# Optimization experiments

Hardware: AMD Instinct MI355X
Metric: run time of the kernel (lower is better)

## Reference

```python
import jax, jax.numpy as jnp
import numpy as np
import math

HIDDEN, HEADS, D_K = 768, 12, 64
BS, SEQ = 4, 2048


def setup_inputs() -> dict:
    key = jax.random.key(0)
    ks = jax.random.split(key, 5)
    s = 1.0 / math.sqrt(HIDDEN)
    return {
        "x": jax.random.normal(ks[0], (BS, SEQ, HIDDEN), dtype=jnp.float32),
        "Wq": jax.random.normal(ks[1], (HIDDEN, HIDDEN), dtype=jnp.float32) * s,
        "bq": jnp.zeros((HIDDEN,), jnp.float32),
        "Wk": jax.random.normal(ks[2], (HIDDEN, HIDDEN), dtype=jnp.float32) * s,
        "bk": jnp.zeros((HIDDEN,), jnp.float32),
        "Wv": jax.random.normal(ks[3], (HIDDEN, HIDDEN), dtype=jnp.float32) * s,
        "bv": jnp.zeros((HIDDEN,), jnp.float32),
        "Wo": jax.random.normal(ks[4], (HIDDEN, HIDDEN), dtype=jnp.float32) * s,
        "bo": jnp.zeros((HIDDEN,), jnp.float32),
    }


def reference(x, Wq, bq, Wk, bk, Wv, bv, Wo, bo):
    bs, seq, _ = x.shape
    # projections; nn.Linear computes x @ W.T + b
    def proj(W, b):
        y = jnp.einsum("bsd,ed->bse", x, W) + b
        return y.reshape(bs, seq, HEADS, D_K).transpose(0, 2, 1, 3)  # [b,h,s,d]
    q, k, v = proj(Wq, bq), proj(Wk, bk), proj(Wv, bv)
    scores = jnp.einsum("bhqd,bhkd->bhqk", q, k) / jnp.sqrt(jnp.float32(D_K))
    attn = jax.nn.softmax(scores, axis=-1)  # dropout = 0 (eval)
    ctx = jnp.einsum("bhqk,bhkd->bhqd", attn, v)
    ctx = ctx.transpose(0, 2, 1, 3).reshape(bs, seq, HIDDEN)
    return jnp.einsum("bsd,ed->bse", ctx, Wo) + bo
```

## Files before the change

kernel.cpp:

```cpp
#include <hip/hip_runtime.h>
#include <hip/hip_bf16.h>

#define HID 768
#define NHEAD 12
#define DKH 64
#define BSZ 4
#define SEQ 2048
#define MTOT (BSZ*SEQ)
#define NBH (BSZ*NHEAD)

typedef __attribute__((ext_vector_type(8))) short   s16x8;
typedef __attribute__((ext_vector_type(8))) __bf16  bf16x8;
typedef __attribute__((ext_vector_type(4))) __bf16  bf16x4;
typedef __attribute__((ext_vector_type(4))) float   f32x4;

#define MFMA16x32(A,B,C) __builtin_amdgcn_mfma_f32_16x16x32_bf16((A),(B),(C),0,0,0)

__device__ __forceinline__ unsigned short f2bf(float f) {
  union { float f; unsigned int u; } a; a.f = f;
  return (unsigned short)((a.u + 0x7FFFu + ((a.u >> 16) & 1u)) >> 16);
}

__device__ __forceinline__ void gload_lds16(const unsigned short* g, unsigned short* l) {
  __builtin_amdgcn_global_load_lds((const __attribute__((address_space(1))) void*)g,
                                   (__attribute__((address_space(3))) void*)l, 16, 0, 0);
}

__global__ __launch_bounds__(256) void cvtall_kernel(const float* __restrict__ x,
                                                     const float* __restrict__ w0,
                                                     const float* __restrict__ w1,
                                                     const float* __restrict__ w2,
                                                     const float* __restrict__ w3,
                                                     unsigned short* __restrict__ xb,
                                                     unsigned short* __restrict__ wb) {
  const int bid = blockIdx.x;
  const float* src; unsigned short* dst; int off;
  if (bid < 6144) {
    src = x; dst = xb; off = bid * 1024;
  } else {
    const int t = bid - 6144;
    const int wi = t / 576;
    const int ro = t - wi * 576;
    src = (wi == 0) ? w0 : (wi == 1) ? w1 : (wi == 2) ? w2 : w3;
    dst = wb + (size_t)wi * HID * HID;
    off = ro * 1024;
  }
  const int i = off + threadIdx.x * 4;
  float4 v = *(const float4*)(src + i);
  ushort4 o;
  o.x = f2bf(v.x); o.y = f2bf(v.y); o.z = f2bf(v.z); o.w = f2bf(v.w);
  *(ushort4*)(dst + i) = o;
}

#define GEMM_STEP(CUR, KTN, DOPREF)                                         \
  {                                                                         \
    if (DOPREF) {                                                           \
      _Pragma("unroll")                                                     \
      for (int i = 0; i < 4; ++i) {                                         \
        const int c = wave * 4 + i;                                         \
        gload_lds16(Aptr + (size_t)(c*8 + sr) * HID + (KTN) + sc8,          \
                    As[(CUR)^1] + c*512);                                   \
      }                                                                     \
      _Pragma("unroll")                                                     \
      for (int i = 0; i < NB; ++i) {                                        \
        const int c = wave * NB + i;                                        \
        gload_lds16(Wptr + (size_t)(c*8 + sr) * HID + (KTN) + sc8,          \
                    Bs[(CUR)^1] + c*512);                                   \
      }                                                                     \
    }                                                                       \
    const char* ab = (const char*)As[CUR];                                  \
    const char* bb = (const char*)Bs[CUR];                                  \
    _Pragma("unroll")                                                       \
    for (int kk = 0; kk < 2; ++kk) {                                        \
      bf16x8 af[4], bfr[NB];                                                \
      _Pragma("unroll")                                                     \
      for (int mb = 0; mb < 4; ++mb) {                                      \
        const int r = wm + mb*16 + l16;                                     \
        af[mb] = *(const bf16x8*)(ab + r*128 + (((kk*4 + lg) ^ (l16 & 7)) << 4)); \
      }                                                                     \
      _Pragma("unroll")                                                     \
      for (int nb = 0; nb < NB; ++nb) {                                     \
        const int r = wn + nb*16 + l16;                                     \
        bfr[nb] = *(const bf16x8*)(bb + r*128 + (((kk*4 + lg) ^ (l16 & 7)) << 4)); \
      }                                                                     \
      _Pragma("unroll")                                                     \
      for (int mb = 0; mb < 4; ++mb)                                        \
        _Pragma("unroll")                                                   \
        for (int nb = 0; nb < NB; ++nb)                                     \
          acc[mb][nb] = MFMA16x32(af[mb], bfr[nb], acc[mb][nb]);            \
    }                                                                       \
    __syncthreads();                                                        \
  }

template<int MODE, int NB>
__global__ __launch_bounds__(256) void gemm_kernel(
    const unsigned short* __restrict__ A,
    const unsigned short* __restrict__ W,
    const float* __restrict__ bias0,
    const float* __restrict__ bias1,
    const float* __restrict__ bias2,
    void* __restrict__ out_raw,
    unsigned short* __restrict__ vtimg)
{
  __shared__ unsigned short As[2][128*64];
  __shared__ unsigned short Bs[2][NB*32*64];
  const int tid  = threadIdx.x;
  const int wave = tid >> 6, lane = tid & 63;
  const int l16  = lane & 15, lg = lane >> 4;
  const int f    = blockIdx.x;
  const int xcd  = f & 7, rr = f >> 3;
  const int bx   = xcd*8 + (rr & 7), by = rr >> 3;
  const int m0   = bx * 128, n0 = by * (NB*32);
  const int wm   = (wave & 1) * 64,  wn = (wave >> 1) * (NB*16);

  const f32x4 z4 = {0.f, 0.f, 0.f, 0.f};
  f32x4 acc[4][NB];
#pragma unroll
  for (int i = 0; i < 4; ++i)
#pragma unroll
    for (int j = 0; j < NB; ++j) acc[i][j] = z4;

  const int sr  = lane >> 3;
  const int sc8 = ((lane & 7) ^ sr) << 3;
  const unsigned short* Aptr = A + (size_t)m0 * HID;
  const unsigned short* Wptr = W + (size_t)n0 * HID;

#pragma unroll
  for (int i = 0; i < 4; ++i) {
    const int c = wave * 4 + i;
    gload_lds16(Aptr + (size_t)(c*8 + sr) * HID + sc8, As[0] + c*512);
  }
#pragma unroll
  for (int i = 0; i < NB; ++i) {
    const int c = wave * NB + i;
    gload_lds16(Wptr + (size_t)(c*8 + sr) * HID + sc8, Bs[0] + c*512);
  }
  __syncthreads();

#pragma unroll 1
  for (int tt = 0; tt < 6; ++tt) {
    GEMM_STEP(0, (2*tt+1)*64, true)
    GEMM_STEP(1, (2*tt+2)*64, (tt < 5))
  }

  if (MODE == 0) {
    unsigned short* out = (unsigned short*)out_raw;
    const float QSCALE = 0.18033688011112042f;
    const int which = (n0 + wn) / HID;
    if (which == 2) {
      const int h = (n0 + wn - 2*HID) >> 6;
#pragma unroll
      for (int nb = 0; nb < NB; ++nb) {
        const int d = nb*16 + l16;
        const float bias = bias2[h*64 + d];
#pragma unroll
        for (int mb = 0; mb < 4; ++mb) {
          const int m    = m0 + wm + mb*16 + lg*4;
          const int b    = m >> 11, s = m & (SEQ - 1);
          const int tile = s >> 6;
          const int slot = ((s & 63) >> 2) ^ l16;
          ushort4 w;
          w.x = f2bf(acc[mb][nb][0] + bias);
          w.y = f2bf(acc[mb][nb][1] + bias);
          w.z = f2bf(acc[mb][nb][2] + bias);
          w.w = f2bf(acc[mb][nb][3] + bias);
          *(ushort4*)(vtimg + ((((size_t)(b*NHEAD + h)*32 + tile)*64 + d)*64 + slot*4)) = w;
        }
      }
    } else {
      const float* bp  = (which == 0) ? bias0 : bias1;
      const float scl  = (which == 0) ? QSCALE : 1.0f;
      const int e_base = n0 + wn - which*HID;
#pragma unroll
      for (int nb = 0; nb < NB; ++nb) {
        const int e = e_base + nb*16 + l16;
        const float bias = bp[e];
        const int h = e >> 6, d = e & 63;
#pragma unroll
        for (int mb = 0; mb < 4; ++mb)
#pragma unroll
          for (int j = 0; j < 4; ++j) {
            const int m = m0 + wm + mb*16 + lg*4 + j;
            const int b = m >> 11, s = m & (SEQ - 1);
            const float v = (acc[mb][nb][j] + bias) * scl;
            out[((((size_t)which*BSZ + b)*NHEAD + h)*SEQ + s)*DKH + d] = f2bf(v);
          }
      }
    }
  } else {
    float* out = (float*)out_raw;
#pragma unroll
    for (int nb = 0; nb < NB; ++nb) {
      const int n = n0 + wn + nb*16 + l16;
      const float bias = bias0[n];
#pragma unroll
      for (int mb = 0; mb < 4; ++mb)
#pragma unroll
        for (int j = 0; j < 4; ++j) {
          const int m = m0 + wm + mb*16 + lg*4 + j;
          out[(size_t)m*HID + n] = acc[mb][nb][j] + bias;
        }
    }
  }
}

#define ATTN_STEP(CUR, DOPREF)                                              \
  {                                                                         \
    if (DOPREF) {                                                           \
      gload_lds16(kSrc0, Ks[(CUR)^1] + wave*1024);                          \
      gload_lds16(kSrc1, Ks[(CUR)^1] + wave*1024 + 512);                    \
      gload_lds16(vSrc0, Vs[(CUR)^1] + wave*1024);                          \
      gload_lds16(vSrc1, Vs[(CUR)^1] + wave*1024 + 512);                    \
      kSrc0 += 64*DKH; kSrc1 += 64*DKH; vSrc0 += 4096; vSrc1 += 4096;       \
    }                                                                       \
    const char* kb = (const char*)Ks[CUR];                                  \
    const char* vb = (const char*)Vs[CUR];                                  \
    f32x4 sc[2][4];                                                         \
    __builtin_amdgcn_s_setprio(1);                                          \
    _Pragma("unroll")                                                       \
    for (int nb = 0; nb < 4; ++nb) {                                        \
      bf16x8 kf0 = *(const bf16x8*)(kb + kbase0 + nb*2048);                 \
      bf16x8 kf1 = *(const bf16x8*)(kb + kbase1 + nb*2048);                 \
      f32x4 z0 = z4, z1 = z4;                                               \
      z0 = MFMA16x32(kf0, qf[0][0], z0);                                    \
      z0 = MFMA16x32(kf1, qf[0][1], z0);                                    \
      z1 = MFMA16x32(kf0, qf[1][0], z1);                                    \
      z1 = MFMA16x32(kf1, qf[1][1], z1);                                    \
      sc[0][nb] = z0; sc[1][nb] = z1;                                       \
    }                                                                       \
    __builtin_amdgcn_s_setprio(0);                                          \
    bf16x8 pa[2][2];                                                        \
    _Pragma("unroll")                                                       \
    for (int qa = 0; qa < 2; ++qa)                                          \
      _Pragma("unroll")                                                     \
      for (int nb = 0; nb < 4; ++nb)                                        \
        _Pragma("unroll")                                                   \
        for (int j = 0; j < 4; ++j)                                         \
          pa[qa][nb>>1][(nb&1)*4 + j] =                                     \
            (__bf16)__builtin_amdgcn_exp2f(sc[qa][nb][j]);                  \
    __builtin_amdgcn_s_setprio(1);                                          \
    csum[0] = MFMA16x32(pa[0][0], ones, csum[0]);                           \
    csum[0] = MFMA16x32(pa[0][1], ones, csum[0]);                           \
    csum[1] = MFMA16x32(pa[1][0], ones, csum[1]);                           \
    csum[1] = MFMA16x32(pa[1][1], ones, csum[1]);                           \
    _Pragma("unroll")                                                       \
    for (int db = 0; db < 4; ++db) {                                        \
      bf16x4 v00 = *(const bf16x4*)(vb + vbase0 + db*2048);                 \
      bf16x4 v01 = *(const bf16x4*)(vb + vbase1 + db*2048);                 \
      bf16x4 v10 = *(const bf16x4*)(vb + vbase2 + db*2048);                 \
      bf16x4 v11 = *(const bf16x4*)(vb + vbase3 + db*2048);                 \
      bf16x8 vf0 = __builtin_shufflevector(v00, v01, 0,1,2,3,4,5,6,7);      \
      bf16x8 vf1 = __builtin_shufflevector(v10, v11, 0,1,2,3,4,5,6,7);      \
      cacc[0][db] = MFMA16x32(pa[0][0], vf0, cacc[0][db]);                  \
      cacc[0][db] = MFMA16x32(pa[0][1], vf1, cacc[0][db]);                  \
      cacc[1][db] = MFMA16x32(pa[1][0], vf0, cacc[1][db]);                  \
      cacc[1][db] = MFMA16x32(pa[1][1], vf1, cacc[1][db]);                  \
    }                                                                       \
    __builtin_amdgcn_s_setprio(0);                                          \
    __syncthreads();                                                        \
  }

__global__ __launch_bounds__(256, 3) void attn_kernel(const unsigned short* __restrict__ qkv,
                                                      const unsigned short* __restrict__ vtimg,
                                                      unsigned short* __restrict__ ctx)
{
  __shared__ unsigned short Ks[2][64*64];
  __shared__ unsigned short Vs[2][64*64];
  const int tid  = threadIdx.x;
  const int wave = tid >> 6, lane = tid & 63;
  const int l16  = lane & 15, lg = lane >> 4;
  const int f   = blockIdx.x;
  const int xcd = f & 7, idx = f >> 3;
  const int bh  = xcd * 6 + (idx >> 4);
  const int qt  = idx & 15;
  const int b   = bh / NHEAD, h = bh - b * NHEAD;
  const int q0  = qt * 128 + wave * 32;

  const unsigned short* Qg = qkv + (size_t)bh * (SEQ*DKH);
  const unsigned short* Kg = qkv + (size_t)(NBH + bh) * (SEQ*DKH);

  const int srow  = lane >> 3;
  const int scolK = ((lane & 7) ^ srow) << 3;
  const unsigned short* kSrc0 = Kg + (size_t)(wave*16 + srow) * DKH + scolK;
  const unsigned short* kSrc1 = Kg + (size_t)(wave*16 + 8 + srow) * DKH + scolK;
  const unsigned short* vSrc0 = vtimg + ((size_t)bh*32*64 + wave*16 + srow) * 64 + (lane & 7) * 8;
  const unsigned short* vSrc1 = vSrc0 + 8*64;

  const int kbase0 = l16*128 + ((lg ^ (l16 & 7)) << 4);
  const int kbase1 = l16*128 + (((lg + 4) ^ (l16 & 7)) << 4);
  const int vbase0 = l16*128 + (((lg     ) ^ l16) << 3);
  const int vbase1 = l16*128 + (((lg +  4) ^ l16) << 3);
  const int vbase2 = l16*128 + (((lg +  8) ^ l16) << 3);
  const int vbase3 = l16*128 + (((lg + 12) ^ l16) << 3);

  bf16x8 qf[2][2];
#pragma unroll
  for (int qa = 0; qa < 2; ++qa) {
    qf[qa][0] = *(const bf16x8*)(Qg + (size_t)(q0 + qa*16 + l16)*DKH + lg*8);
    qf[qa][1] = *(const bf16x8*)(Qg + (size_t)(q0 + qa*16 + l16)*DKH + 32 + lg*8);
  }

  bf16x8 ones;
#pragma unroll
  for (int e = 0; e < 8; ++e) ones[e] = (__bf16)1.0f;

  const f32x4 z4 = {0.f,0.f,0.f,0.f};
  f32x4 cacc[2][4];
  f32x4 csum[2] = {z4, z4};
#pragma unroll
  for (int qa = 0; qa < 2; ++qa)
#pragma unroll
    for (int db = 0; db < 4; ++db) cacc[qa][db] = z4;

  gload_lds16(kSrc0, Ks[0] + wave*1024);
  gload_lds16(kSrc1, Ks[0] + wave*1024 + 512);
  gload_lds16(vSrc0, Vs[0] + wave*1024);
  gload_lds16(vSrc1, Vs[0] + wave*1024 + 512);
  kSrc0 += 64*DKH; kSrc1 += 64*DKH; vSrc0 += 4096; vSrc1 += 4096;
  __syncthreads();

#pragma unroll 1
  for (int tt = 0; tt < 16; ++tt) {
    ATTN_STEP(0, true)
    ATTN_STEP(1, (tt < 15))
  }

#pragma unroll
  for (int qa = 0; qa < 2; ++qa) {
    f32x4 inv;
#pragma unroll
    for (int j = 0; j < 4; ++j) inv[j] = 1.0f / csum[qa][j];
#pragma unroll
    for (int db = 0; db < 4; ++db)
#pragma unroll
      for (int j = 0; j < 4; ++j) {
        const int srow2 = q0 + qa*16 + lg*4 + j;
        ctx[((size_t)(b*SEQ + srow2))*HID + h*DKH + db*16 + l16] = f2bf(cacc[qa][db][j] * inv[j]);
      }
  }
}

extern "C" void kernel_launch(void* const* d_in, const int* in_sizes, int n_in,
                              void* d_out, int out_size, void* d_ws, size_t ws_size,
                              hipStream_t stream) {
  (void)in_sizes; (void)n_in; (void)out_size; (void)ws_size;
  const float* x  = (const float*)d_in[0];
  const float* Wq = (const float*)d_in[1];
  const float* bq = (const float*)d_in[2];
  const float* Wk = (const float*)d_in[3];
  const float* bk = (const float*)d_in[4];
  const float* Wv = (const float*)d_in[5];
  const float* bv = (const float*)d_in[6];
  const float* Wo = (const float*)d_in[7];
  const float* bo = (const float*)d_in[8];

  unsigned short* ws   = (unsigned short*)d_ws;
  unsigned short* Xb   = ws;
  unsigned short* Wqkv = Xb + (size_t)MTOT * HID;
  unsigned short* Wob  = Wqkv + (size_t)3 * HID * HID;
  unsigned short* qkvb = Wob + (size_t)HID * HID;
  unsigned short* vtb  = qkvb + (size_t)2 * NBH * SEQ * DKH;
  unsigned short* ctxb = Xb;

  cvtall_kernel<<<6144 + 4*576, 256, 0, stream>>>(x, Wq, Wk, Wv, Wo, Xb, Wqkv);

  gemm_kernel<0,4><<<1152, 256, 0, stream>>>(Xb, Wqkv, bq, bk, bv, qkvb, vtb);
  attn_kernel<<<768, 256, 0, stream>>>(qkvb, vtb, ctxb);
  gemm_kernel<1,2><<<768, 256, 0, stream>>>(ctxb, Wob, bo, nullptr, nullptr, d_out, nullptr);
}
```

Before: 126.8 us.

## Give QKV GEMM a triple-buffered K=32 pipeline with vmcnt-based waits

```diff
diff --git a/kernel.cpp b/kernel.cpp
--- a/kernel.cpp
+++ b/kernel.cpp
@@ -52,73 +52,208 @@
   *(ushort4*)(dst + i) = o;
 }
 
-#define GEMM_STEP(CUR, KTN, DOPREF)                                         \
-  {                                                                         \
-    if (DOPREF) {                                                           \
-      _Pragma("unroll")                                                     \
-      for (int i = 0; i < 4; ++i) {                                         \
-        const int c = wave * 4 + i;                                         \
-        gload_lds16(Aptr + (size_t)(c*8 + sr) * HID + (KTN) + sc8,          \
-                    As[(CUR)^1] + c*512);                                   \
-      }                                                                     \
-      _Pragma("unroll")                                                     \
-      for (int i = 0; i < NB; ++i) {                                        \
-        const int c = wave * NB + i;                                        \
-        gload_lds16(Wptr + (size_t)(c*8 + sr) * HID + (KTN) + sc8,          \
-                    Bs[(CUR)^1] + c*512);                                   \
-      }                                                                     \
-    }                                                                       \
-    const char* ab = (const char*)As[CUR];                                  \
-    const char* bb = (const char*)Bs[CUR];                                  \
+#define VM4 asm volatile("s_waitcnt vmcnt(4)" ::: "memory")
+#define VM0 asm volatile("s_waitcnt vmcnt(0)" ::: "memory")
+#define CFENCE asm volatile("" ::: "memory")
+
+#define G0_STAGE(BUF, KTN)                                                  \
     _Pragma("unroll")                                                       \
-    for (int kk = 0; kk < 2; ++kk) {                                        \
-      bf16x8 af[4], bfr[NB];                                                \
+    for (int i = 0; i < 2; ++i) {                                           \
+      const int c = wave * 2 + i;                                           \
+      gload_lds16(Aptr + (size_t)(c*16 + sr4) * HID + (KTN) + sc4,          \
+                  As[BUF] + c*512);                                         \
+      gload_lds16(Wptr + (size_t)(c*16 + sr4) * HID + (KTN) + sc4,          \
+                  Bs[BUF] + c*512);                                         \
+    }
+
+#define G0_COMPUTE(BUF)                                                     \
+    {                                                                       \
+      const char* ab = (const char*)As[BUF];                                \
+      const char* bb = (const char*)Bs[BUF];                                \
+      bf16x8 af[4], bfr[4];                                                 \
       _Pragma("unroll")                                                     \
       for (int mb = 0; mb < 4; ++mb) {                                      \
         const int r = wm + mb*16 + l16;                                     \
-        af[mb] = *(const bf16x8*)(ab + r*128 + (((kk*4 + lg) ^ (l16 & 7)) << 4)); \
-      }                                                                     \
-      _Pragma("unroll")                                                     \
-      for (int nb = 0; nb < NB; ++nb) {                                     \
+        af[mb] = *(const bf16x8*)(ab + r*64 + (((lg) ^ (r & 3)) << 4));     \
+      }                                                                     \
+      _Pragma("unroll")                                                     \
+      for (int nb = 0; nb < 4; ++nb) {                                      \
         const int r = wn + nb*16 + l16;                                     \
-        bfr[nb] = *(const bf16x8*)(bb + r*128 + (((kk*4 + lg) ^ (l16 & 7)) << 4)); \
+        bfr[nb] = *(const bf16x8*)(bb + r*64 + (((lg) ^ (r & 3)) << 4));    \
       }                                                                     \
       _Pragma("unroll")                                                     \
       for (int mb = 0; mb < 4; ++mb)                                        \
         _Pragma("unroll")                                                   \
-        for (int nb = 0; nb < NB; ++nb)                                     \
+        for (int nb = 0; nb < 4; ++nb)                                      \
           acc[mb][nb] = MFMA16x32(af[mb], bfr[nb], acc[mb][nb]);            \
-    }                                                                       \
-    __syncthreads();                                                        \
-  }
-
-template<int MODE, int NB>
-__global__ __launch_bounds__(256) void gemm_kernel(
+    }
+
+#define G0_STEP(BUF, KTN, PF)                                               \
+  {                                                                         \
+    if (PF) { G0_STAGE(((BUF)+2)%3, KTN) }                                  \
+    G0_COMPUTE(BUF)                                                         \
+    if (PF) { VM4; } else { VM0; }                                          \
+    __builtin_amdgcn_sched_barrier(0);                                      \
+    __builtin_amdgcn_s_barrier();                                           \
+    CFENCE;                                                                 \
+  }
+
+__global__ __launch_bounds__(256, 3) void gemm0_kernel(
     const unsigned short* __restrict__ A,
     const unsigned short* __restrict__ W,
     const float* __restrict__ bias0,
     const float* __restrict__ bias1,
     const float* __restrict__ bias2,
-    void* __restrict__ out_raw,
+    unsigned short* __restrict__ out,
     unsigned short* __restrict__ vtimg)
 {
-  __shared__ unsigned short As[2][128*64];
-  __shared__ unsigned short Bs[2][NB*32*64];
+  __shared__ unsigned short As[3][128*32];
+  __shared__ unsigned short Bs[3][128*32];
   const int tid  = threadIdx.x;
   const int wave = tid >> 6, lane = tid & 63;
   const int l16  = lane & 15, lg = lane >> 4;
   const int f    = blockIdx.x;
   const int xcd  = f & 7, rr = f >> 3;
   const int bx   = xcd*8 + (rr & 7), by = rr >> 3;
-  const int m0   = bx * 128, n0 = by * (NB*32);
-  const int wm   = (wave & 1) * 64,  wn = (wave >> 1) * (NB*16);
+  const int m0   = bx * 128, n0 = by * 128;
+  const int wm   = (wave & 1) * 64,  wn = (wave >> 1) * 64;
 
   const f32x4 z4 = {0.f, 0.f, 0.f, 0.f};
-  f32x4 acc[4][NB];
+  f32x4 acc[4][4];
 #pragma unroll
   for (int i = 0; i < 4; ++i)
 #pragma unroll
-    for (int j = 0; j < NB; ++j) acc[i][j] = z4;
+    for (int j = 0; j < 4; ++j) acc[i][j] = z4;
+
+  const int sr4 = lane >> 2;
+  const int sc4 = ((lane & 3) ^ (sr4 & 3)) << 3;
+  const unsigned short* Aptr = A + (size_t)m0 * HID;
+  const unsigned short* Wptr = W + (size_t)n0 * HID;
+
+  G0_STAGE(0, 0)
+  G0_STAGE(1, 32)
+  VM4;
+  __builtin_amdgcn_sched_barrier(0);
+  __builtin_amdgcn_s_barrier();
+  CFENCE;
+
+#pragma unroll 1
+  for (int tt = 0; tt < 7; ++tt) {
+    G0_STEP(0, (tt*3+2)*32, 1)
+    G0_STEP(1, (tt*3+3)*32, 1)
+    G0_STEP(2, (tt*3+4)*32, 1)
+  }
+  G0_STEP(0, 23*32, 1)
+  G0_STEP(1, 0, 0)
+  G0_COMPUTE(2)
+
+  const float QSCALE = 0.18033688011112042f;
+  const int which = (n0 + wn) / HID;
+  if (which == 2) {
+    const int h = (n0 + wn - 2*HID) >> 6;
+#pragma unroll
+    for (int nb = 0; nb < 4; ++nb) {
+      const int d = nb*16 + l16;
+      const float bias = bias2[h*64 + d];
+#pragma unroll
+      for (int mb = 0; mb < 4; ++mb) {
+        const int m    = m0 + wm + mb*16 + lg*4;
+        const int b    = m >> 11, s = m & (SEQ - 1);
+        const int tile = s >> 6;
+        const int slot = ((s & 63) >> 2) ^ l16;
+        ushort4 w;
+        w.x = f2bf(acc[mb][nb][0] + bias);
+        w.y = f2bf(acc[mb][nb][1] + bias);
+        w.z = f2bf(acc[mb][nb][2] + bias);
+        w.w = f2bf(acc[mb][nb][3] + bias);
+        *(ushort4*)(vtimg + ((((size_t)(b*NHEAD + h)*32 + tile)*64 + d)*64 + slot*4)) = w;
+      }
+    }
+  } else {
+    const float* bp  = (which == 0) ? bias0 : bias1;
+    const float scl  = (which == 0) ? QSCALE : 1.0f;
+    const int e_base = n0 + wn - which*HID;
+#pragma unroll
+    for (int nb = 0; nb < 4; ++nb) {
+      const int e = e_base + nb*16 + l16;
+      const float bias = bp[e];
+      const int h = e >> 6, d = e & 63;
+#pragma unroll
+      for (int mb = 0; mb < 4; ++mb)
+#pragma unroll
+        for (int j = 0; j < 4; ++j) {
+          const int m = m0 + wm + mb*16 + lg*4 + j;
+          const int b = m >> 11, s = m & (SEQ - 1);
+          const float v = (acc[mb][nb][j] + bias) * scl;
+          out[((((size_t)which*BSZ + b)*NHEAD + h)*SEQ + s)*DKH + d] = f2bf(v);
+        }
+    }
+  }
+}
+
+#define GEMM_STEP(CUR, KTN, DOPREF)                                         \
+  {                                                                         \
+    if (DOPREF) {                                                           \
+      _Pragma("unroll")                                                     \
+      for (int i = 0; i < 4; ++i) {                                         \
+        const int c = wave * 4 + i;                                         \
+        gload_lds16(Aptr + (size_t)(c*8 + sr) * HID + (KTN) + sc8,          \
+                    As[(CUR)^1] + c*512);                                   \
+      }                                                                     \
+      _Pragma("unroll")                                                     \
+      for (int i = 0; i < 2; ++i) {                                         \
+        const int c = wave * 2 + i;                                         \
+        gload_lds16(Wptr + (size_t)(c*8 + sr) * HID + (KTN) + sc8,          \
+                    Bs[(CUR)^1] + c*512);                                   \
+      }                                                                     \
+    }                                                                       \
+    const char* ab = (const char*)As[CUR];                                  \
+    const char* bb = (const char*)Bs[CUR];                                  \
+    _Pragma("unroll")                                                       \
+    for (int kk = 0; kk < 2; ++kk) {                                        \
+      bf16x8 af[4], bfr[2];                                                 \
+      _Pragma("unroll")                                                     \
+      for (int mb = 0; mb < 4; ++mb) {                                      \
+        const int r = wm + mb*16 + l16;                                     \
+        af[mb] = *(const bf16x8*)(ab + r*128 + (((kk*4 + lg) ^ (l16 & 7)) << 4)); \
+      }                                                                     \
+      _Pragma("unroll")                                                     \
+      for (int nb = 0; nb < 2; ++nb) {                                      \
+        const int r = wn + nb*16 + l16;                                     \
+        bfr[nb] = *(const bf16x8*)(bb + r*128 + (((kk*4 + lg) ^ (l16 & 7)) << 4)); \
+      }                                                                     \
+      _Pragma("unroll")                                                     \
+      for (int mb = 0; mb < 4; ++mb)                                        \
+        _Pragma("unroll")                                                   \
+        for (int nb = 0; nb < 2; ++nb)                                      \
+          acc[mb][nb] = MFMA16x32(af[mb], bfr[nb], acc[mb][nb]);            \
+    }                                                                       \
+    __syncthreads();                                                        \
+  }
+
+__global__ __launch_bounds__(256) void gemm1_kernel(
+    const unsigned short* __restrict__ A,
+    const unsigned short* __restrict__ W,
+    const float* __restrict__ bias0,
+    float* __restrict__ out)
+{
+  __shared__ unsigned short As[2][128*64];
+  __shared__ unsigned short Bs[2][64*64];
+  const int tid  = threadIdx.x;
+  const int wave = tid >> 6, lane = tid & 63;
+  const int l16  = lane & 15, lg = lane >> 4;
+  const int f    = blockIdx.x;
+  const int xcd  = f & 7, rr = f >> 3;
+  const int bx   = xcd*8 + (rr & 7), by = rr >> 3;
+  const int m0   = bx * 128, n0 = by * 64;
+  const int wm   = (wave & 1) * 64,  wn = (wave >> 1) * 32;
+
+  const f32x4 z4 = {0.f, 0.f, 0.f, 0.f};
+  f32x4 acc[4][2];
+#pragma unroll
+  for (int i = 0; i < 4; ++i)
+#pragma unroll
+    for (int j = 0; j < 2; ++j) acc[i][j] = z4;
 
   const int sr  = lane >> 3;
   const int sc8 = ((lane & 7) ^ sr) << 3;
@@ -131,8 +266,8 @@
     gload_lds16(Aptr + (size_t)(c*8 + sr) * HID + sc8, As[0] + c*512);
   }
 #pragma unroll
-  for (int i = 0; i < NB; ++i) {
-    const int c = wave * NB + i;
+  for (int i = 0; i < 2; ++i) {
+    const int c = wave * 2 + i;
     gload_lds16(Wptr + (size_t)(c*8 + sr) * HID + sc8, Bs[0] + c*512);
   }
   __syncthreads();
@@ -143,64 +278,17 @@
     GEMM_STEP(1, (2*tt+2)*64, (tt < 5))
   }
 
-  if (MODE == 0) {
-    unsigned short* out = (unsigned short*)out_raw;
-    const float QSCALE = 0.18033688011112042f;
-    const int which = (n0 + wn) / HID;
-    if (which == 2) {
-      const int h = (n0 + wn - 2*HID) >> 6;
-#pragma unroll
-      for (int nb = 0; nb < NB; ++nb) {
-        const int d = nb*16 + l16;
-        const float bias = bias2[h*64 + d];
-#pragma unroll
-        for (int mb = 0; mb < 4; ++mb) {
-          const int m    = m0 + wm + mb*16 + lg*4;
-          const int b    = m >> 11, s = m & (SEQ - 1);
-          const int tile = s >> 6;
-          const int slot = ((s & 63) >> 2) ^ l16;
-          ushort4 w;
-          w.x = f2bf(acc[mb][nb][0] + bias);
-          w.y = f2bf(acc[mb][nb][1] + bias);
-          w.z = f2bf(acc[mb][nb][2] + bias);
-          w.w = f2bf(acc[mb][nb][3] + bias);
-          *(ushort4*)(vtimg + ((((size_t)(b*NHEAD + h)*32 + tile)*64 + d)*64 + slot*4)) = w;
-        }
+#pragma unroll
+  for (int nb = 0; nb < 2; ++nb) {
+    const int n = n0 + wn + nb*16 + l16;
+    const float bias = bias0[n];
+#pragma unroll
+    for (int mb = 0; mb < 4; ++mb)
+#pragma unroll
+      for (int j = 0; j < 4; ++j) {
+        const int m = m0 + wm + mb*16 + lg*4 + j;
+        out[(size_t)m*HID + n] = acc[mb][nb][j] + bias;
       }
-    } else {
-      const float* bp  = (which == 0) ? bias0 : bias1;
-      const float scl  = (which == 0) ? QSCALE : 1.0f;
-      const int e_base = n0 + wn - which*HID;
-#pragma unroll
-      for (int nb = 0; nb < NB; ++nb) {
-        const int e = e_base + nb*16 + l16;
-        const float bias = bp[e];
-        const int h = e >> 6, d = e & 63;
-#pragma unroll
-        for (int mb = 0; mb < 4; ++mb)
-#pragma unroll
-          for (int j = 0; j < 4; ++j) {
-            const int m = m0 + wm + mb*16 + lg*4 + j;
-            const int b = m >> 11, s = m & (SEQ - 1);
-            const float v = (acc[mb][nb][j] + bias) * scl;
-            out[((((size_t)which*BSZ + b)*NHEAD + h)*SEQ + s)*DKH + d] = f2bf(v);
-          }
-      }
-    }
-  } else {
-    float* out = (float*)out_raw;
-#pragma unroll
-    for (int nb = 0; nb < NB; ++nb) {
-      const int n = n0 + wn + nb*16 + l16;
-      const float bias = bias0[n];
-#pragma unroll
-      for (int mb = 0; mb < 4; ++mb)
-#pragma unroll
-        for (int j = 0; j < 4; ++j) {
-          const int m = m0 + wm + mb*16 + lg*4 + j;
-          out[(size_t)m*HID + n] = acc[mb][nb][j] + bias;
-        }
-    }
   }
 }
 
@@ -364,7 +452,7 @@
 
   cvtall_kernel<<<6144 + 4*576, 256, 0, stream>>>(x, Wq, Wk, Wv, Wo, Xb, Wqkv);
 
-  gemm_kernel<0,4><<<1152, 256, 0, stream>>>(Xb, Wqkv, bq, bk, bv, qkvb, vtb);
+  gemm0_kernel<<<1152, 256, 0, stream>>>(Xb, Wqkv, bq, bk, bv, qkvb, vtb);
   attn_kernel<<<768, 256, 0, stream>>>(qkvb, vtb, ctxb);
-  gemm_kernel<1,2><<<768, 256, 0, stream>>>(ctxb, Wob, bo, nullptr, nullptr, d_out, nullptr);
-}
+  gemm1_kernel<<<768, 256, 0, stream>>>(ctxb, Wob, bo, (float*)d_out);
+}
```

New measurement: 126.1 us. Within noise of the previous version (-0.5%).
